# Optimization experiments

Measured on AMD Instinct MI355X. Metric: run time of the kernel, lower is better.

The kernel has to match this reference:

```python
import jax, jax.numpy as jnp
import numpy as np

B, T, D, H = 4, 2048, 1024, 16
HD = D // H  # head_dim = 64


def setup_inputs() -> dict:
    key = jax.random.key(0)
    k1, k2, k3 = jax.random.split(key, 3)
    x = jax.random.normal(k1, (B, T, D), dtype=jnp.float32)
    # rotary cache: (T, head_dim/2, 2) holding (cos, sin)
    inv_freq = 1.0 / (10000.0 ** (jnp.arange(0, HD, 2, dtype=jnp.float32) / HD))  # (HD/2,)
    t = jnp.arange(T, dtype=jnp.float32)
    freqs = jnp.einsum('t,f->tf', t, inv_freq)  # (T, HD/2)
    rope = jnp.stack([jnp.cos(freqs), jnp.sin(freqs)], axis=-1)  # (T, HD/2, 2)
    # causal boolean attn mask, broadcastable (1,1,T,T)
    mask = jnp.tril(jnp.ones((T, T), dtype=bool))[None, None]
    # params (bias-free linears), scaled like nn.Linear default init
    W_attn = jax.random.normal(k2, (3 * D, D), dtype=jnp.float32) / np.sqrt(D)
    W_proj = jax.random.normal(k3, (D, D), dtype=jnp.float32) / np.sqrt(D)
    return {"x": x, "rope": rope, "mask": mask, "W_attn": W_attn, "W_proj": W_proj}


def apply_rope(x, rope):
    # x: (B, T, H, HD); rope: (T, HD/2, 2)
    b, t, h, hd = x.shape
    xr = x.reshape(b, t, h, hd // 2, 2)
    x1, x2 = xr[..., 0], xr[..., 1]
    cos = rope[None, :, None, :, 0]  # (1, T, 1, HD/2)
    sin = rope[None, :, None, :, 1]
    out = jnp.stack([x1 * cos - x2 * sin, x1 * sin + x2 * cos], axis=-1)
    return out.reshape(b, t, h, hd)


def reference(x, rope, mask, W_attn, W_proj):
    b, t, d = x.shape
    qkv = jnp.einsum('btd,ed->bte', x, W_attn)  # (B, T, 3D)
    q, k, v = jnp.split(qkv, 3, axis=2)
    q = apply_rope(q.reshape(b, t, H, HD), rope)
    k = apply_rope(k.reshape(b, t, H, HD), rope)
    v = v.reshape(b, t, H, HD)
    # (B, H, T, HD)
    q = q.transpose(0, 2, 1, 3)
    k = k.transpose(0, 2, 1, 3)
    v = v.transpose(0, 2, 1, 3)
    scale = 1.0 / np.sqrt(HD)
    scores = jnp.einsum('bhqd,bhkd->bhqk', q, k) * scale
    scores = jnp.where(mask, scores, jnp.finfo(scores.dtype).min)
    attn = jax.nn.softmax(scores, axis=-1)
    o = jnp.einsum('bhqk,bhkd->bhqd', attn, v)
    o = o.transpose(0, 2, 1, 3).reshape(b, t, d)
    return jnp.einsum('btd,ed->bte', o, W_proj)
```

## Files before the change

### kernel.cpp

```cpp
#include <hip/hip_runtime.h>

typedef unsigned short u16;
typedef unsigned int u32;
typedef unsigned long long u64;
typedef __bf16 v8bf __attribute__((ext_vector_type(8)));
typedef __bf16 v4bf __attribute__((ext_vector_type(4)));
typedef float v4f __attribute__((ext_vector_type(4)));
typedef float v16f __attribute__((ext_vector_type(16)));
typedef u32 v4u __attribute__((ext_vector_type(4)));

#define BB 4
#define TT 2048
#define HH 16
#define DD 1024

__device__ __forceinline__ u16 f2bf(float f){
  u32 u = __float_as_uint(f);
  u32 r = u + 0x7FFFu + ((u >> 16) & 1u);
  return (u16)(r >> 16);
}
__device__ __forceinline__ float bf2f(u16 h){ return __uint_as_float(((u32)h) << 16); }
__device__ __forceinline__ v16f z16(){
  v16f z;
#pragma unroll
  for (int i = 0; i < 16; i++) z[i] = 0.f;
  return z;
}
__device__ __forceinline__ u32 cvtpk(float lo, float hi){
  u32 d;
  asm("v_cvt_pk_bf16_f32 %0, %1, %2" : "=v"(d) : "v"(lo), "v"(hi));
  return d;
}
__device__ __forceinline__ void swap32(u32 &a, u32 &b){
  asm volatile("v_permlane32_swap_b32 %0, %1" : "+v"(a), "+v"(b));
}

typedef __attribute__((address_space(1))) const void gas_t;
typedef __attribute__((address_space(3))) void las_t;
__device__ __forceinline__ void gl_lds16(const void* g, void* l){
  __builtin_amdgcn_global_load_lds((gas_t*)g, (las_t*)l, 16, 0, 0);
}

__global__ __launch_bounds__(256) void k_convert(
    const float* __restrict__ x, const float* __restrict__ wa,
    const float* __restrict__ wp, u16* __restrict__ xb,
    u16* __restrict__ wab, u16* __restrict__ wpb){
  int i = blockIdx.x * 256 + threadIdx.x;
  const int nxq = (BB*TT*DD) / 4;
  const int naq = (3*DD*DD) / 4;
  const float* src; u16* dst; int j;
  if (i < nxq)            { src = x;  dst = xb;  j = i; }
  else if (i < nxq + naq) { src = wa; dst = wab; j = i - nxq; }
  else                    { src = wp; dst = wpb; j = i - nxq - naq; }
  float4 v = reinterpret_cast<const float4*>(src)[j];
  u64 p = (u64)f2bf(v.x) | ((u64)f2bf(v.y) << 16)
        | ((u64)f2bf(v.z) << 32) | ((u64)f2bf(v.w) << 48);
  reinterpret_cast<u64*>(dst)[j] = p;
}

__global__ __launch_bounds__(256) void k_gemm_bt(
    const u16* __restrict__ A, const u16* __restrict__ Bt,
    int M, int N, int K, int mode, float* __restrict__ Cf,
    u16* __restrict__ qo, u16* __restrict__ ko, u16* __restrict__ vo){
  __shared__ char smem[32768];
  char* As = smem;
  char* Bs = smem + 16384;
  const int t = threadIdx.x;
  const int lane = t & 63, w = t >> 6;
  const int c = lane & 15, g = lane >> 4;
  const int nbn = N >> 7;
  const int bm = blockIdx.x / nbn, bn = blockIdx.x % nbn;
  const long arow0 = (long)bm * 128;
  const long brow0 = (long)bn * 128;
  const int wrow = (w >> 1) * 64, wcol = (w & 1) * 64;

  v4f acc[4][4];
#pragma unroll
  for (int i = 0; i < 4; i++)
#pragma unroll
    for (int j = 0; j < 4; j++){ v4f z = {0.f,0.f,0.f,0.f}; acc[i][j] = z; }

  for (int k0 = 0; k0 < K; k0 += 64){
    __syncthreads();
#pragma unroll
    for (int i = 0; i < 4; i++){
      int slot = t + i * 256;
      int row  = slot >> 3;
      int cb   = (slot & 7) << 4;
      int scb  = cb ^ ((row & 7) << 4);
      gl_lds16((const char*)A  + ((arow0 + row) * (long)K + k0) * 2 + scb,
               As + ((t & 192) + i * 256) * 16);
      gl_lds16((const char*)Bt + ((brow0 + row) * (long)K + k0) * 2 + scb,
               Bs + ((t & 192) + i * 256) * 16);
    }
    __syncthreads();

    v8bf af[4][2], bfr[4][2];
#pragma unroll
    for (int mt = 0; mt < 4; mt++){
      int row = wrow + mt * 16 + c;
      int sw  = (row & 7) << 4;
#pragma unroll
      for (int ks = 0; ks < 2; ks++)
        af[mt][ks] = *(const v8bf*)(As + row * 128 + ((ks * 64 + g * 16) ^ sw));
    }
#pragma unroll
    for (int nt = 0; nt < 4; nt++){
      int row = wcol + nt * 16 + c;
      int sw  = (row & 7) << 4;
#pragma unroll
      for (int ks = 0; ks < 2; ks++)
        bfr[nt][ks] = *(const v8bf*)(Bs + row * 128 + ((ks * 64 + g * 16) ^ sw));
    }
#pragma unroll
    for (int mt = 0; mt < 4; mt++)
#pragma unroll
      for (int nt = 0; nt < 4; nt++)
#pragma unroll
        for (int ks = 0; ks < 2; ks++)
          acc[mt][nt] = __builtin_amdgcn_mfma_f32_16x16x32_bf16(
              af[mt][ks], bfr[nt][ks], acc[mt][nt], 0, 0, 0);
  }

  if (mode == 1){
#pragma unroll
    for (int mt = 0; mt < 4; mt++)
#pragma unroll
      for (int nt = 0; nt < 4; nt++)
#pragma unroll
        for (int r = 0; r < 4; r++){
          long row = arow0 + wrow + mt * 16 + g * 4 + r;
          long col = brow0 + wcol + nt * 16 + c;
          Cf[row * N + col] = acc[mt][nt][r];
        }
  } else {
    long bb = arow0 >> 11;
#pragma unroll
    for (int mt = 0; mt < 4; mt++)
#pragma unroll
      for (int nt = 0; nt < 4; nt++){
        int e    = (int)brow0 + wcol + nt * 16 + c;
        int tsel = e >> 10;
        int h    = (e >> 6) & 15;
        int d    = e & 63;
        long tpos = (arow0 & 2047) + wrow + mt * 16 + g * 4;
        if (tsel == 2){
          v4bf pk;
#pragma unroll
          for (int r = 0; r < 4; r++) pk[r] = (__bf16)acc[mt][nt][r];
          *(v4bf*)(vo + (((bb * HH + h) * 64 + d) << 11) + tpos) = pk;
        } else {
          u16* dst = tsel ? ko : qo;
#pragma unroll
          for (int r = 0; r < 4; r++)
            dst[((bb * HH + h) * TT + tpos + r) * 64 + d] = f2bf(acc[mt][nt][r]);
        }
      }
  }
}

__global__ __launch_bounds__(256) void k_rope2(
    u16* __restrict__ qb, u16* __restrict__ kb, const float* __restrict__ rope){
  int tid   = blockIdx.x * 256 + threadIdx.x;
  int which = tid >> 20;
  int r     = tid & 1048575;
  int s     = r & 7;
  int row   = r >> 3;
  int tpos  = row & 2047;
  u16* base = (which ? kb : qb) + (long)row * 64 + s * 8;
  int4 w0 = *(const int4*)base;
  float4 r01 = *(const float4*)(rope + tpos * 64 + s * 8);
  float4 r23 = *(const float4*)(rope + tpos * 64 + s * 8 + 4);
  float cs[4] = {r01.x, r01.z, r23.x, r23.z};
  float sn[4] = {r01.y, r01.w, r23.y, r23.w};
  float scale = which ? 1.0f : 0.18033688011112042f;
  int wv[4] = {w0.x, w0.y, w0.z, w0.w};
  int ov[4];
#pragma unroll
  for (int j = 0; j < 4; j++){
    float x1 = bf2f((u16)((u32)wv[j] & 0xffffu));
    float x2 = bf2f((u16)((u32)wv[j] >> 16));
    float oe = (x1 * cs[j] - x2 * sn[j]) * scale;
    float od = (x1 * sn[j] + x2 * cs[j]) * scale;
    ov[j] = (int)((u32)f2bf(oe) | ((u32)f2bf(od) << 16));
  }
  int4 out = {ov[0], ov[1], ov[2], ov[3]};
  *(int4*)base = out;
}

__global__ __launch_bounds__(256) void k_attn(
    const u16* __restrict__ Q, const u16* __restrict__ K,
    const u16* __restrict__ Vt, u16* __restrict__ O){
  __shared__ char smem[16384];
  char* ksm = smem;
  char* vsm = smem + 8192;
  int bx = blockIdx.x;
  int bh = bx & 63;
  int bt = 15 - (bx >> 6);
  int q0 = bt * 128;
  int b = bh >> 4, h = bh & 15;
  const u16* Qb = Q  + (size_t)bh * TT * 64;
  const u16* Kb = K  + (size_t)bh * TT * 64;
  const u16* Vb = Vt + (size_t)bh * 64 * TT;
  const int t = threadIdx.x, lane = t & 63, w = t >> 6;
  const int c = lane & 31, hi = lane >> 5;
  const int swz = (c & 7) << 4;
  const int wq0 = q0 + w * 32;

  v8bf qf[4];
  {
    const u16* qrow = Qb + (size_t)(wq0 + c) * 64 + hi * 8;
#pragma unroll
    for (int kc = 0; kc < 4; kc++) qf[kc] = *(const v8bf*)(qrow + kc * 16);
  }

  float m_ = -1e30f, l_ = 0.f;
  v16f accO0 = z16(), accO1 = z16();

  for (int kv0 = 0; kv0 < q0 + 128; kv0 += 64){
    __syncthreads();
#pragma unroll
    for (int i = 0; i < 2; i++){
      int s   = t + i * 256;
      int row = s >> 3;
      int cb  = (s & 7) << 4;
      int scb = cb ^ ((row & 7) << 4);
      gl_lds16((const char*)Kb + (size_t)(kv0 + row) * 128 + scb,
               ksm + ((t & 192) + i * 256) * 16);
      gl_lds16((const char*)Vb + (size_t)row * (TT * 2) + (size_t)kv0 * 2 + scb,
               vsm + ((t & 192) + i * 256) * 16);
    }
    __syncthreads();

    if (kv0 <= wq0 + 31){
      v16f s0 = z16(), s1 = z16();
      __builtin_amdgcn_s_setprio(1);
#pragma unroll
      for (int kc = 0; kc < 4; kc++){
        int off = (kc * 32 + hi * 16) ^ swz;
        v8bf a0 = *(const v8bf*)(ksm + c * 128 + off);
        v8bf a1 = *(const v8bf*)(ksm + (32 + c) * 128 + off);
        s0 = __builtin_amdgcn_mfma_f32_32x32x16_bf16(a0, qf[kc], s0, 0, 0, 0);
        s1 = __builtin_amdgcn_mfma_f32_32x32x16_bf16(a1, qf[kc], s1, 0, 0, 0);
      }
      __builtin_amdgcn_s_setprio(0);
      if (kv0 + 63 > wq0){
        int q = wq0 + c;
#pragma unroll
        for (int r = 0; r < 16; r++){
          int crow = (r & 3) + 8 * (r >> 2) + 4 * hi;
          if (kv0 + crow > q)      s0[r] = -1e30f;
          if (kv0 + 32 + crow > q) s1[r] = -1e30f;
        }
      }
      float mx = -1e30f;
#pragma unroll
      for (int r = 0; r < 16; r++){ mx = fmaxf(mx, s0[r]); mx = fmaxf(mx, s1[r]); }
      mx = fmaxf(mx, __shfl_xor(mx, 32, 64));
      if (!__all(mx <= m_)){
        float mn = fmaxf(m_, mx);
        float alpha = __builtin_amdgcn_exp2f(m_ - mn);
        m_ = mn;
        l_ *= alpha;
#pragma unroll
        for (int r = 0; r < 16; r++){ accO0[r] *= alpha; accO1[r] *= alpha; }
      }
      float sum = 0.f;
#pragma unroll
      for (int r = 0; r < 16; r++){
        float p0 = __builtin_amdgcn_exp2f(s0[r] - m_);
        float p1 = __builtin_amdgcn_exp2f(s1[r] - m_);
        s0[r] = p0; s1[r] = p1;
        sum += p0 + p1;
      }
      sum += __shfl_xor(sum, 32, 64);
      l_ += sum;
      v8bf pbf[4];
      {
        u32 wd[16];
#pragma unroll
        for (int i = 0; i < 8; i++) wd[i]     = cvtpk(s0[2*i], s0[2*i+1]);
#pragma unroll
        for (int i = 0; i < 8; i++) wd[8 + i] = cvtpk(s1[2*i], s1[2*i+1]);
        swap32(wd[0], wd[2]);  swap32(wd[1], wd[3]);
        swap32(wd[4], wd[6]);  swap32(wd[5], wd[7]);
        swap32(wd[8], wd[10]); swap32(wd[9], wd[11]);
        swap32(wd[12], wd[14]); swap32(wd[13], wd[15]);
        v4u u0 = {wd[0], wd[1], wd[2], wd[3]};
        v4u u1 = {wd[4], wd[5], wd[6], wd[7]};
        v4u u2 = {wd[8], wd[9], wd[10], wd[11]};
        v4u u3 = {wd[12], wd[13], wd[14], wd[15]};
        pbf[0] = __builtin_bit_cast(v8bf, u0);
        pbf[1] = __builtin_bit_cast(v8bf, u1);
        pbf[2] = __builtin_bit_cast(v8bf, u2);
        pbf[3] = __builtin_bit_cast(v8bf, u3);
      }
      __builtin_amdgcn_s_setprio(1);
#pragma unroll
      for (int kc = 0; kc < 4; kc++){
        int off = (kc * 32 + hi * 16) ^ swz;
        v8bf va0 = *(const v8bf*)(vsm + c * 128 + off);
        v8bf va1 = *(const v8bf*)(vsm + (32 + c) * 128 + off);
        accO0 = __builtin_amdgcn_mfma_f32_32x32x16_bf16(va0, pbf[kc], accO0, 0, 0, 0);
        accO1 = __builtin_amdgcn_mfma_f32_32x32x16_bf16(va1, pbf[kc], accO1, 0, 0, 0);
      }
      __builtin_amdgcn_s_setprio(0);
    }
  }

  float inv = __builtin_amdgcn_rcpf(l_);
  int q = wq0 + c;
  u16* orow = O + ((size_t)(b * TT + q)) * DD + h * 64;
#pragma unroll
  for (int q4 = 0; q4 < 4; q4++){
    v4bf o0, o1;
#pragma unroll
    for (int j = 0; j < 4; j++){
      o0[j] = (__bf16)(accO0[q4 * 4 + j] * inv);
      o1[j] = (__bf16)(accO1[q4 * 4 + j] * inv);
    }
    *(v4bf*)(orow + q4 * 8 + hi * 4)      = o0;
    *(v4bf*)(orow + 32 + q4 * 8 + hi * 4) = o1;
  }
}

extern "C" void kernel_launch(void* const* d_in, const int* in_sizes, int n_in,
                              void* d_out, int out_size, void* d_ws, size_t ws_size,
                              hipStream_t stream){
  const float* x    = (const float*)d_in[0];
  const float* rope = (const float*)d_in[1];
  const float* Wa   = (const float*)d_in[3];
  const float* Wp   = (const float*)d_in[4];

  char* ws = (char*)d_ws;
  u16* xb  = (u16*)(ws);
  u16* wab = (u16*)(ws + (16u << 20));
  u16* wpb = (u16*)(ws + (22u << 20));
  u16* qb  = (u16*)(ws + (24u << 20));
  u16* kb  = (u16*)(ws + (40u << 20));
  u16* vtb = (u16*)(ws + (56u << 20));
  u16* ob  = xb;

  k_convert<<<dim3(12288), dim3(256), 0, stream>>>(x, Wa, Wp, xb, wab, wpb);
  k_gemm_bt<<<dim3(24 * 64), dim3(256), 0, stream>>>(
      xb, wab, 8192, 3072, 1024, 0, nullptr, qb, kb, vtb);
  k_rope2<<<dim3(8192), dim3(256), 0, stream>>>(qb, kb, rope);
  k_attn<<<dim3(1024), dim3(256), 0, stream>>>(qb, kb, vtb, ob);
  k_gemm_bt<<<dim3(8 * 64), dim3(256), 0, stream>>>(
      ob, wpb, 8192, 1024, 1024, 1, (float*)d_out, nullptr, nullptr, nullptr);
}
```

Before: 176.7 us.

## Add 256x256 double-buffered QKV GEMM kernel with interleaved prefetch and block swizzle

Replaces the 128x128 single-buffered QKV projection GEMM with a new 512-thread kernel that computes 256x256 tiles. It double-buffers LDS (128KB) and interleaves the global-to-LDS prefetch of the next K step between MFMA quarters, with priority raised around the MFMA blocks. Workgroup IDs are swizzled so neighbouring blocks share input tiles in cache. The goal is more data reuse per load and better overlap of memory with MFMA. The cost is far higher LDS and register use, with only 384 workgroups, which may leave some CUs idle.

```diff
diff --git a/kernel.cpp b/kernel.cpp
--- a/kernel.cpp
+++ b/kernel.cpp
@@ -40,6 +40,11 @@
 __device__ __forceinline__ void gl_lds16(const void* g, void* l){
   __builtin_amdgcn_global_load_lds((gas_t*)g, (las_t*)l, 16, 0, 0);
 }
+
+#define WAIT_LGKM0 do{ asm volatile("s_waitcnt lgkmcnt(0)" ::: "memory"); \
+                       __builtin_amdgcn_sched_barrier(0); }while(0)
+#define WAIT_VM0   do{ asm volatile("s_waitcnt vmcnt(0)" ::: "memory"); \
+                       __builtin_amdgcn_sched_barrier(0); }while(0)
 
 __global__ __launch_bounds__(256) void k_convert(
     const float* __restrict__ x, const float* __restrict__ wa,
@@ -58,10 +63,148 @@
   reinterpret_cast<u64*>(dst)[j] = p;
 }
 
+__global__ __launch_bounds__(512, 2) void k_gemm256(
+    const u16* __restrict__ A, const u16* __restrict__ Bt,
+    int M, int N, int K,
+    u16* __restrict__ qo, u16* __restrict__ ko, u16* __restrict__ vo){
+  __shared__ char smem[131072];
+  char* Abase = smem;
+  char* Bbase = smem + 65536;
+  const int t = threadIdx.x;
+  const int lane = t & 63, w = t >> 6;
+  const int wm = w >> 2, wn = w & 3;
+  const int c = lane & 15, g = lane >> 4;
+  const int nbn = N >> 8;
+  const int nwg = gridDim.x;
+  int swzb = (blockIdx.x & 7) * (nwg >> 3) + (blockIdx.x >> 3);
+  const int bm = swzb / nbn, bn = swzb % nbn;
+  const long arow0 = (long)bm * 256;
+  const long bcol0 = (long)bn * 256;
+  const long strA = (long)K * 2;
+
+  v4f acc[8][4];
+#pragma unroll
+  for (int i = 0; i < 8; i++)
+#pragma unroll
+    for (int j = 0; j < 4; j++){ v4f z = {0.f,0.f,0.f,0.f}; acc[i][j] = z; }
+
+  const int ldsw = (t & 448) * 16;
+
+#define STAGEH(GSRC, GROW0, LDST, H, K0) do{                                   \
+  _Pragma("unroll")                                                            \
+  for (int l = 0; l < 2; l++){                                                 \
+    int slot = t + l * 512;                                                    \
+    int row  = slot >> 3;                                                      \
+    int scb  = ((slot & 7) << 4) ^ ((row & 7) << 4);                           \
+    gl_lds16((const char*)(GSRC) + ((GROW0) + (H)*128 + row) * strA + (K0)*2 + scb, \
+             (LDST) + (H)*16384 + l*8192 + ldsw);                              \
+  } }while(0)
+
+  v8bf a[4][2], b[4][2];
+
+#define LDA(MH, ACUR) do{                                                      \
+  _Pragma("unroll")                                                            \
+  for (int mi = 0; mi < 4; mi++){                                              \
+    int row = wm*128 + ((MH)*4+mi)*16 + c;                                     \
+    int sw  = (row & 7) << 4;                                                  \
+    _Pragma("unroll")                                                          \
+    for (int ks = 0; ks < 2; ks++)                                             \
+      a[mi][ks] = *(const v8bf*)((ACUR) + row*128 + ((ks*64 + g*16) ^ sw));    \
+  } }while(0)
+
+#define LDB(BCUR) do{                                                          \
+  _Pragma("unroll")                                                            \
+  for (int n = 0; n < 4; n++){                                                 \
+    int row = wn*64 + n*16 + c;                                                \
+    int sw  = (row & 7) << 4;                                                  \
+    _Pragma("unroll")                                                          \
+    for (int ks = 0; ks < 2; ks++)                                             \
+      b[n][ks] = *(const v8bf*)((BCUR) + row*128 + ((ks*64 + g*16) ^ sw));     \
+  } }while(0)
+
+#define MFMA_QUAD(MH, NH) do{                                                  \
+  __builtin_amdgcn_s_setprio(1);                                               \
+  _Pragma("unroll")                                                            \
+  for (int mi = 0; mi < 4; mi++)                                               \
+    _Pragma("unroll")                                                          \
+    for (int ni = 0; ni < 2; ni++)                                             \
+      _Pragma("unroll")                                                        \
+      for (int ks = 0; ks < 2; ks++)                                           \
+        acc[(MH)*4+mi][(NH)*2+ni] = __builtin_amdgcn_mfma_f32_16x16x32_bf16(   \
+            a[mi][ks], b[(NH)*2+ni][ks], acc[(MH)*4+mi][(NH)*2+ni], 0, 0, 0);  \
+  __builtin_amdgcn_s_setprio(0); }while(0)
+
+  const int nsteps = K >> 6;
+
+  STAGEH(A, arow0, Abase, 0, 0);
+  STAGEH(A, arow0, Abase, 1, 0);
+  STAGEH(Bt, bcol0, Bbase, 0, 0);
+  STAGEH(Bt, bcol0, Bbase, 1, 0);
+  WAIT_VM0;
+  __builtin_amdgcn_s_barrier();
+
+  for (int ts = 0; ts < nsteps; ++ts){
+    char* Acur = Abase + (ts & 1) * 32768;
+    char* Bcur = Bbase + (ts & 1) * 32768;
+    char* Anxt = Abase + ((ts & 1) ^ 1) * 32768;
+    char* Bnxt = Bbase + ((ts & 1) ^ 1) * 32768;
+    const int k1 = (ts + 1) << 6;
+    const bool pf = (ts + 1 < nsteps);
+
+    LDA(0, Acur); LDB(Bcur);
+    if (pf) STAGEH(A, arow0, Anxt, 0, k1);
+    __builtin_amdgcn_s_barrier();
+    WAIT_LGKM0;
+    MFMA_QUAD(0, 0);
+    __builtin_amdgcn_s_barrier();
+    if (pf) STAGEH(A, arow0, Anxt, 1, k1);
+    __builtin_amdgcn_s_barrier();
+    MFMA_QUAD(0, 1);
+    __builtin_amdgcn_s_barrier();
+    LDA(1, Acur);
+    if (pf) STAGEH(Bt, bcol0, Bnxt, 0, k1);
+    __builtin_amdgcn_s_barrier();
+    WAIT_LGKM0;
+    MFMA_QUAD(1, 0);
+    __builtin_amdgcn_s_barrier();
+    if (pf) STAGEH(Bt, bcol0, Bnxt, 1, k1);
+    __builtin_amdgcn_s_barrier();
+    MFMA_QUAD(1, 1);
+    WAIT_VM0;
+    __builtin_amdgcn_s_barrier();
+  }
+
+  long bb = arow0 >> 11;
+#pragma unroll
+  for (int m = 0; m < 8; m++)
+#pragma unroll
+    for (int n = 0; n < 4; n++){
+      int e    = (int)bcol0 + wn * 64 + n * 16 + c;
+      int tsel = e >> 10;
+      int hh   = (e >> 6) & 15;
+      int d    = e & 63;
+      long tpos = (arow0 & 2047) + wm * 128 + m * 16 + g * 4;
+      if (tsel == 2){
+        v4bf pk;
+#pragma unroll
+        for (int r = 0; r < 4; r++) pk[r] = (__bf16)acc[m][n][r];
+        *(v4bf*)(vo + (((bb * HH + hh) * 64 + d) << 11) + tpos) = pk;
+      } else {
+        u16* dst = tsel ? ko : qo;
+#pragma unroll
+        for (int r = 0; r < 4; r++)
+          dst[((bb * HH + hh) * TT + tpos + r) * 64 + d] = f2bf(acc[m][n][r]);
+      }
+    }
+#undef STAGEH
+#undef LDA
+#undef LDB
+#undef MFMA_QUAD
+}
+
 __global__ __launch_bounds__(256) void k_gemm_bt(
     const u16* __restrict__ A, const u16* __restrict__ Bt,
-    int M, int N, int K, int mode, float* __restrict__ Cf,
-    u16* __restrict__ qo, u16* __restrict__ ko, u16* __restrict__ vo){
+    int M, int N, int K, float* __restrict__ Cf){
   __shared__ char smem[32768];
   char* As = smem;
   char* Bs = smem + 16384;
@@ -122,41 +265,16 @@
               af[mt][ks], bfr[nt][ks], acc[mt][nt], 0, 0, 0);
   }
 
-  if (mode == 1){
-#pragma unroll
-    for (int mt = 0; mt < 4; mt++)
-#pragma unroll
-      for (int nt = 0; nt < 4; nt++)
-#pragma unroll
-        for (int r = 0; r < 4; r++){
-          long row = arow0 + wrow + mt * 16 + g * 4 + r;
-          long col = brow0 + wcol + nt * 16 + c;
-          Cf[row * N + col] = acc[mt][nt][r];
-        }
-  } else {
-    long bb = arow0 >> 11;
-#pragma unroll
-    for (int mt = 0; mt < 4; mt++)
-#pragma unroll
-      for (int nt = 0; nt < 4; nt++){
-        int e    = (int)brow0 + wcol + nt * 16 + c;
-        int tsel = e >> 10;
-        int h    = (e >> 6) & 15;
-        int d    = e & 63;
-        long tpos = (arow0 & 2047) + wrow + mt * 16 + g * 4;
-        if (tsel == 2){
-          v4bf pk;
-#pragma unroll
-          for (int r = 0; r < 4; r++) pk[r] = (__bf16)acc[mt][nt][r];
-          *(v4bf*)(vo + (((bb * HH + h) * 64 + d) << 11) + tpos) = pk;
-        } else {
-          u16* dst = tsel ? ko : qo;
-#pragma unroll
-          for (int r = 0; r < 4; r++)
-            dst[((bb * HH + h) * TT + tpos + r) * 64 + d] = f2bf(acc[mt][nt][r]);
-        }
-      }
-  }
+#pragma unroll
+  for (int mt = 0; mt < 4; mt++)
+#pragma unroll
+    for (int nt = 0; nt < 4; nt++)
+#pragma unroll
+      for (int r = 0; r < 4; r++){
+        long row = arow0 + wrow + mt * 16 + g * 4 + r;
+        long col = brow0 + wcol + nt * 16 + c;
+        Cf[row * N + col] = acc[mt][nt][r];
+      }
 }
 
 __global__ __launch_bounds__(256) void k_rope2(
@@ -342,10 +460,10 @@
   u16* ob  = xb;
 
   k_convert<<<dim3(12288), dim3(256), 0, stream>>>(x, Wa, Wp, xb, wab, wpb);
-  k_gemm_bt<<<dim3(24 * 64), dim3(256), 0, stream>>>(
-      xb, wab, 8192, 3072, 1024, 0, nullptr, qb, kb, vtb);
+  k_gemm256<<<dim3(32 * 12), dim3(512), 0, stream>>>(
+      xb, wab, 8192, 3072, 1024, qb, kb, vtb);
   k_rope2<<<dim3(8192), dim3(256), 0, stream>>>(qb, kb, rope);
   k_attn<<<dim3(1024), dim3(256), 0, stream>>>(qb, kb, vtb, ob);
   k_gemm_bt<<<dim3(8 * 64), dim3(256), 0, stream>>>(
-      ob, wpb, 8192, 1024, 1024, 1, (float*)d_out, nullptr, nullptr, nullptr);
-}
+      ob, wpb, 8192, 1024, 1024, (float*)d_out);
+}
```

New measurement: 184.5 us. 1.04x slower.

## Fuse RoPE into a larger 256x192-tile double-buffered QKV GEMM

Applied to the files above, without the earlier changes.

Replaces the 128x128 QKV projection GEMM and the separate RoPE kernel with a 512-thread kernel that uses 256x192 tiles. The kernel double-buffers A/B in LDS with direct global-to-LDS loads, raises MFMA priority during compute, and swizzles the block order. RoPE and the Q scale are applied in the epilogue using a rope slice staged in LDS and a lane shuffle to fetch the pair partner. This removes the separate read-modify-write pass over Q/K and one launch, but uses 112KB of LDS per block, which limits occupancy, and the epilogue stores remain scalar bf16.

```diff
diff --git a/kernel.cpp b/kernel.cpp
--- a/kernel.cpp
+++ b/kernel.cpp
@@ -40,6 +40,11 @@
 __device__ __forceinline__ void gl_lds16(const void* g, void* l){
   __builtin_amdgcn_global_load_lds((gas_t*)g, (las_t*)l, 16, 0, 0);
 }
+
+#define WAIT_LGKM0 do{ asm volatile("s_waitcnt lgkmcnt(0)" ::: "memory"); \
+                       __builtin_amdgcn_sched_barrier(0); }while(0)
+#define WAIT_VM0   do{ asm volatile("s_waitcnt vmcnt(0)" ::: "memory"); \
+                       __builtin_amdgcn_sched_barrier(0); }while(0)
 
 __global__ __launch_bounds__(256) void k_convert(
     const float* __restrict__ x, const float* __restrict__ wa,
@@ -58,10 +63,159 @@
   reinterpret_cast<u64*>(dst)[j] = p;
 }
 
+__global__ __launch_bounds__(512, 2) void k_gemm256(
+    const u16* __restrict__ A, const u16* __restrict__ Bt,
+    const float* __restrict__ rope,
+    u16* __restrict__ qo, u16* __restrict__ ko, u16* __restrict__ vo){
+  __shared__ char smem[114688];
+  char* Ab = smem;
+  char* Bb = smem + 65536;
+  const int t = threadIdx.x, lane = t & 63;
+  const int w = t >> 6, wm = w >> 2, wn = w & 3;
+  const int c = lane & 15, g = lane >> 4;
+  const int swzb = (blockIdx.x & 7) * 64 + (blockIdx.x >> 3);
+  const int bm = swzb >> 4, bn = swzb & 15;
+  const long arow0 = (long)bm * 256;
+  const int  bcol0 = bn * 192;
+  const int  ldsw = (t & 448) * 16;
+
+  v4f acc[8][3];
+#pragma unroll
+  for (int i = 0; i < 8; i++)
+#pragma unroll
+    for (int j = 0; j < 3; j++){ v4f z = {0.f,0.f,0.f,0.f}; acc[i][j] = z; }
+
+#pragma unroll
+  for (int l = 0; l < 4; l++){
+    int slot = t + l * 512, row = slot >> 3;
+    int scb = ((slot & 7) << 4) ^ ((row & 7) << 4);
+    gl_lds16((const char*)A + (arow0 + row) * 2048 + scb, Ab + l * 8192 + ldsw);
+  }
+#pragma unroll
+  for (int l = 0; l < 3; l++){
+    int slot = t + l * 512, row = slot >> 3;
+    int scb = ((slot & 7) << 4) ^ ((row & 7) << 4);
+    gl_lds16((const char*)Bt + (bcol0 + row) * 2048 + scb, Bb + l * 8192 + ldsw);
+  }
+
+#pragma unroll 1
+  for (int ts = 0; ts < 16; ++ts){
+    char* Ac = Ab + (ts & 1) * 32768;
+    char* Bc = Bb + (ts & 1) * 24576;
+    WAIT_VM0;
+    __builtin_amdgcn_s_barrier();
+    if (ts + 1 < 16){
+      char* An = Ab + ((ts & 1) ^ 1) * 32768;
+      char* Bn = Bb + ((ts & 1) ^ 1) * 24576;
+      const int k0 = (ts + 1) << 6;
+#pragma unroll
+      for (int l = 0; l < 4; l++){
+        int slot = t + l * 512, row = slot >> 3;
+        int scb = ((slot & 7) << 4) ^ ((row & 7) << 4);
+        gl_lds16((const char*)A + (arow0 + row) * 2048 + k0 * 2 + scb,
+                 An + l * 8192 + ldsw);
+      }
+#pragma unroll
+      for (int l = 0; l < 3; l++){
+        int slot = t + l * 512, row = slot >> 3;
+        int scb = ((slot & 7) << 4) ^ ((row & 7) << 4);
+        gl_lds16((const char*)Bt + (bcol0 + row) * 2048 + k0 * 2 + scb,
+                 Bn + l * 8192 + ldsw);
+      }
+    }
+    v8bf a[4][2], b[3][2];
+#pragma unroll
+    for (int n = 0; n < 3; n++){
+      int row = wn * 48 + n * 16 + c, sw = (row & 7) << 4;
+      b[n][0] = *(const v8bf*)(Bc + row * 128 + ((g * 16) ^ sw));
+      b[n][1] = *(const v8bf*)(Bc + row * 128 + ((64 + g * 16) ^ sw));
+    }
+#pragma unroll
+    for (int mi = 0; mi < 4; mi++){
+      int row = wm * 128 + mi * 16 + c, sw = (row & 7) << 4;
+      a[mi][0] = *(const v8bf*)(Ac + row * 128 + ((g * 16) ^ sw));
+      a[mi][1] = *(const v8bf*)(Ac + row * 128 + ((64 + g * 16) ^ sw));
+    }
+    WAIT_LGKM0;
+    __builtin_amdgcn_s_setprio(1);
+#pragma unroll
+    for (int mi = 0; mi < 4; mi++)
+#pragma unroll
+      for (int n = 0; n < 3; n++)
+#pragma unroll
+        for (int ks = 0; ks < 2; ks++)
+          acc[mi][n] = __builtin_amdgcn_mfma_f32_16x16x32_bf16(
+              a[mi][ks], b[n][ks], acc[mi][n], 0, 0, 0);
+    __builtin_amdgcn_s_setprio(0);
+    __builtin_amdgcn_s_barrier();
+#pragma unroll
+    for (int mi = 0; mi < 4; mi++){
+      int row = wm * 128 + 64 + mi * 16 + c, sw = (row & 7) << 4;
+      a[mi][0] = *(const v8bf*)(Ac + row * 128 + ((g * 16) ^ sw));
+      a[mi][1] = *(const v8bf*)(Ac + row * 128 + ((64 + g * 16) ^ sw));
+    }
+    WAIT_LGKM0;
+    __builtin_amdgcn_s_setprio(1);
+#pragma unroll
+    for (int mi = 0; mi < 4; mi++)
+#pragma unroll
+      for (int n = 0; n < 3; n++)
+#pragma unroll
+        for (int ks = 0; ks < 2; ks++)
+          acc[4 + mi][n] = __builtin_amdgcn_mfma_f32_16x16x32_bf16(
+              a[mi][ks], b[n][ks], acc[4 + mi][n], 0, 0, 0);
+    __builtin_amdgcn_s_setprio(0);
+  }
+
+  __builtin_amdgcn_s_barrier();
+  const long bb  = arow0 >> 11;
+  const int  tq0 = (int)(arow0 & 2047);
+  const bool hasqk = (bcol0 < 2048);
+  if (hasqk){
+#pragma unroll
+    for (int l = 0; l < 8; l++)
+      gl_lds16((const char*)rope + tq0 * 256 + (t + l * 512) * 16,
+               smem + l * 8192 + ldsw);
+    WAIT_VM0;
+  }
+  __builtin_amdgcn_s_barrier();
+
+#pragma unroll
+  for (int m = 0; m < 8; m++){
+    const int tposb = wm * 128 + m * 16 + g * 4;
+#pragma unroll
+    for (int n = 0; n < 3; n++){
+      int e    = bcol0 + wn * 48 + n * 16 + c;
+      int tsel = e >> 10;
+      int hh   = (e >> 6) & 15;
+      int d    = e & 63;
+      if (tsel == 2){
+        v4bf pk;
+#pragma unroll
+        for (int r = 0; r < 4; r++) pk[r] = (__bf16)acc[m][n][r];
+        *(v4bf*)(vo + (((bb * HH + hh) * 64 + d) << 11) + tq0 + tposb) = pk;
+      } else {
+        const float qs = tsel ? 1.0f : 0.18033688011112042f;
+        const int f = d >> 1;
+        const bool odd = d & 1;
+        u16* dst = tsel ? ko : qo;
+        long base = ((bb * HH + hh) * TT + tq0 + tposb) * 64 + d;
+#pragma unroll
+        for (int r = 0; r < 4; r++){
+          float v = acc[m][n][r];
+          float2 cn = *(const float2*)(smem + (tposb + r) * 256 + f * 8);
+          float px = __shfl_xor(v, 1, 64);
+          float o = odd ? (px * cn.y + v * cn.x) : (v * cn.x - px * cn.y);
+          dst[base + (long)r * 64] = f2bf(o * qs);
+        }
+      }
+    }
+  }
+}
+
 __global__ __launch_bounds__(256) void k_gemm_bt(
     const u16* __restrict__ A, const u16* __restrict__ Bt,
-    int M, int N, int K, int mode, float* __restrict__ Cf,
-    u16* __restrict__ qo, u16* __restrict__ ko, u16* __restrict__ vo){
+    int M, int N, int K, float* __restrict__ Cf){
   __shared__ char smem[32768];
   char* As = smem;
   char* Bs = smem + 16384;
@@ -122,70 +276,16 @@
               af[mt][ks], bfr[nt][ks], acc[mt][nt], 0, 0, 0);
   }
 
-  if (mode == 1){
-#pragma unroll
-    for (int mt = 0; mt < 4; mt++)
-#pragma unroll
-      for (int nt = 0; nt < 4; nt++)
-#pragma unroll
-        for (int r = 0; r < 4; r++){
-          long row = arow0 + wrow + mt * 16 + g * 4 + r;
-          long col = brow0 + wcol + nt * 16 + c;
-          Cf[row * N + col] = acc[mt][nt][r];
-        }
-  } else {
-    long bb = arow0 >> 11;
-#pragma unroll
-    for (int mt = 0; mt < 4; mt++)
-#pragma unroll
-      for (int nt = 0; nt < 4; nt++){
-        int e    = (int)brow0 + wcol + nt * 16 + c;
-        int tsel = e >> 10;
-        int h    = (e >> 6) & 15;
-        int d    = e & 63;
-        long tpos = (arow0 & 2047) + wrow + mt * 16 + g * 4;
-        if (tsel == 2){
-          v4bf pk;
-#pragma unroll
-          for (int r = 0; r < 4; r++) pk[r] = (__bf16)acc[mt][nt][r];
-          *(v4bf*)(vo + (((bb * HH + h) * 64 + d) << 11) + tpos) = pk;
-        } else {
-          u16* dst = tsel ? ko : qo;
-#pragma unroll
-          for (int r = 0; r < 4; r++)
-            dst[((bb * HH + h) * TT + tpos + r) * 64 + d] = f2bf(acc[mt][nt][r]);
-        }
-      }
-  }
-}
-
-__global__ __launch_bounds__(256) void k_rope2(
-    u16* __restrict__ qb, u16* __restrict__ kb, const float* __restrict__ rope){
-  int tid   = blockIdx.x * 256 + threadIdx.x;
-  int which = tid >> 20;
-  int r     = tid & 1048575;
-  int s     = r & 7;
-  int row   = r >> 3;
-  int tpos  = row & 2047;
-  u16* base = (which ? kb : qb) + (long)row * 64 + s * 8;
-  int4 w0 = *(const int4*)base;
-  float4 r01 = *(const float4*)(rope + tpos * 64 + s * 8);
-  float4 r23 = *(const float4*)(rope + tpos * 64 + s * 8 + 4);
-  float cs[4] = {r01.x, r01.z, r23.x, r23.z};
-  float sn[4] = {r01.y, r01.w, r23.y, r23.w};
-  float scale = which ? 1.0f : 0.18033688011112042f;
-  int wv[4] = {w0.x, w0.y, w0.z, w0.w};
-  int ov[4];
-#pragma unroll
-  for (int j = 0; j < 4; j++){
-    float x1 = bf2f((u16)((u32)wv[j] & 0xffffu));
-    float x2 = bf2f((u16)((u32)wv[j] >> 16));
-    float oe = (x1 * cs[j] - x2 * sn[j]) * scale;
-    float od = (x1 * sn[j] + x2 * cs[j]) * scale;
-    ov[j] = (int)((u32)f2bf(oe) | ((u32)f2bf(od) << 16));
-  }
-  int4 out = {ov[0], ov[1], ov[2], ov[3]};
-  *(int4*)base = out;
+#pragma unroll
+  for (int mt = 0; mt < 4; mt++)
+#pragma unroll
+    for (int nt = 0; nt < 4; nt++)
+#pragma unroll
+      for (int r = 0; r < 4; r++){
+        long row = arow0 + wrow + mt * 16 + g * 4 + r;
+        long col = brow0 + wcol + nt * 16 + c;
+        Cf[row * N + col] = acc[mt][nt][r];
+      }
 }
 
 __global__ __launch_bounds__(256) void k_attn(
@@ -342,10 +442,8 @@
   u16* ob  = xb;
 
   k_convert<<<dim3(12288), dim3(256), 0, stream>>>(x, Wa, Wp, xb, wab, wpb);
-  k_gemm_bt<<<dim3(24 * 64), dim3(256), 0, stream>>>(
-      xb, wab, 8192, 3072, 1024, 0, nullptr, qb, kb, vtb);
-  k_rope2<<<dim3(8192), dim3(256), 0, stream>>>(qb, kb, rope);
+  k_gemm256<<<dim3(512), dim3(512), 0, stream>>>(xb, wab, rope, qb, kb, vtb);
   k_attn<<<dim3(1024), dim3(256), 0, stream>>>(qb, kb, vtb, ob);
   k_gemm_bt<<<dim3(8 * 64), dim3(256), 0, stream>>>(
-      ob, wpb, 8192, 1024, 1024, 1, (float*)d_out, nullptr, nullptr, nullptr);
-}
+      ob, wpb, 8192, 1024, 1024, (float*)d_out);
+}
```

After: 167.6 us. 1.05x faster.

## Fuse RoPE and query scaling into QKV GEMM epilogue

Applied to the files above, without the earlier changes.

Removes the separate rope kernel and applies rotary embedding and the query scale inside the QKV GEMM epilogue. Rope cos/sin values for the block's 128 positions are staged into shared memory, and each lane gets its rotation partner via a lane-xor shuffle. This avoids an extra full read and write pass over Q and K in global memory plus a launch, at the cost of extra epilogue work and a shared-memory load with barriers.

```diff
diff --git a/kernel.cpp b/kernel.cpp
--- a/kernel.cpp
+++ b/kernel.cpp
@@ -60,6 +60,7 @@
 
 __global__ __launch_bounds__(256) void k_gemm_bt(
     const u16* __restrict__ A, const u16* __restrict__ Bt,
+    const float* __restrict__ rope,
     int M, int N, int K, int mode, float* __restrict__ Cf,
     u16* __restrict__ qo, u16* __restrict__ ko, u16* __restrict__ vo){
   __shared__ char smem[32768];
@@ -134,58 +135,47 @@
           Cf[row * N + col] = acc[mt][nt][r];
         }
   } else {
-    long bb = arow0 >> 11;
-#pragma unroll
-    for (int mt = 0; mt < 4; mt++)
+    const int t0 = (int)(arow0 & 2047);
+    __syncthreads();
+#pragma unroll
+    for (int l = 0; l < 8; l++)
+      gl_lds16((const char*)rope + (size_t)t0 * 256 + (size_t)(t + l * 256) * 16,
+               smem + ((t & 192) + l * 256) * 16);
+    __syncthreads();
+
+    const long bb = arow0 >> 11;
+#pragma unroll
+    for (int mt = 0; mt < 4; mt++){
+      const int tposb = wrow + mt * 16 + g * 4;
 #pragma unroll
       for (int nt = 0; nt < 4; nt++){
         int e    = (int)brow0 + wcol + nt * 16 + c;
         int tsel = e >> 10;
-        int h    = (e >> 6) & 15;
+        int hh   = (e >> 6) & 15;
         int d    = e & 63;
-        long tpos = (arow0 & 2047) + wrow + mt * 16 + g * 4;
         if (tsel == 2){
           v4bf pk;
 #pragma unroll
           for (int r = 0; r < 4; r++) pk[r] = (__bf16)acc[mt][nt][r];
-          *(v4bf*)(vo + (((bb * HH + h) * 64 + d) << 11) + tpos) = pk;
+          *(v4bf*)(vo + (((bb * HH + hh) * 64 + d) << 11) + t0 + tposb) = pk;
         } else {
+          const float qs = tsel ? 1.0f : 0.18033688011112042f;
+          const int f = d >> 1;
+          const bool odd = d & 1;
           u16* dst = tsel ? ko : qo;
-#pragma unroll
-          for (int r = 0; r < 4; r++)
-            dst[((bb * HH + h) * TT + tpos + r) * 64 + d] = f2bf(acc[mt][nt][r]);
+          long base = ((bb * HH + hh) * TT + t0 + tposb) * 64 + d;
+#pragma unroll
+          for (int r = 0; r < 4; r++){
+            float v = acc[mt][nt][r];
+            float2 cn = *(const float2*)(smem + (tposb + r) * 256 + f * 8);
+            float px = __shfl_xor(v, 1, 64);
+            float o = odd ? (px * cn.y + v * cn.x) : (v * cn.x - px * cn.y);
+            dst[base + (long)r * 64] = f2bf(o * qs);
+          }
         }
       }
-  }
-}
-
-__global__ __launch_bounds__(256) void k_rope2(
-    u16* __restrict__ qb, u16* __restrict__ kb, const float* __restrict__ rope){
-  int tid   = blockIdx.x * 256 + threadIdx.x;
-  int which = tid >> 20;
-  int r     = tid & 1048575;
-  int s     = r & 7;
-  int row   = r >> 3;
-  int tpos  = row & 2047;
-  u16* base = (which ? kb : qb) + (long)row * 64 + s * 8;
-  int4 w0 = *(const int4*)base;
-  float4 r01 = *(const float4*)(rope + tpos * 64 + s * 8);
-  float4 r23 = *(const float4*)(rope + tpos * 64 + s * 8 + 4);
-  float cs[4] = {r01.x, r01.z, r23.x, r23.z};
-  float sn[4] = {r01.y, r01.w, r23.y, r23.w};
-  float scale = which ? 1.0f : 0.18033688011112042f;
-  int wv[4] = {w0.x, w0.y, w0.z, w0.w};
-  int ov[4];
-#pragma unroll
-  for (int j = 0; j < 4; j++){
-    float x1 = bf2f((u16)((u32)wv[j] & 0xffffu));
-    float x2 = bf2f((u16)((u32)wv[j] >> 16));
-    float oe = (x1 * cs[j] - x2 * sn[j]) * scale;
-    float od = (x1 * sn[j] + x2 * cs[j]) * scale;
-    ov[j] = (int)((u32)f2bf(oe) | ((u32)f2bf(od) << 16));
-  }
-  int4 out = {ov[0], ov[1], ov[2], ov[3]};
-  *(int4*)base = out;
+    }
+  }
 }
 
 __global__ __launch_bounds__(256) void k_attn(
@@ -343,9 +333,9 @@
 
   k_convert<<<dim3(12288), dim3(256), 0, stream>>>(x, Wa, Wp, xb, wab, wpb);
   k_gemm_bt<<<dim3(24 * 64), dim3(256), 0, stream>>>(
-      xb, wab, 8192, 3072, 1024, 0, nullptr, qb, kb, vtb);
-  k_rope2<<<dim3(8192), dim3(256), 0, stream>>>(qb, kb, rope);
+      xb, wab, rope, 8192, 3072, 1024, 0, nullptr, qb, kb, vtb);
   k_attn<<<dim3(1024), dim3(256), 0, stream>>>(qb, kb, vtb, ob);
   k_gemm_bt<<<dim3(8 * 64), dim3(256), 0, stream>>>(
-      ob, wpb, 8192, 1024, 1024, 1, (float*)d_out, nullptr, nullptr, nullptr);
-}
+      ob, wpb, nullptr, 8192, 1024, 1024, 1, (float*)d_out,
+      nullptr, nullptr, nullptr);
+}
```

After: 170.4 us. 3.6% less time.
